# Kernel tuning notes

Hardware: AMD Instinct MI355X
Metric: run time of the kernel (lower is better)

## Reference

```python
import jax, jax.numpy as jnp
import numpy as np

B, N, DIM, H, D = 1, 1024, 512, 8, 64
BC, BS, K, W = 16, 16, 8, 256   # compress blk, selection blk, top-k blocks, sliding window
C = N // BC                     # number of compression / selection blocks
SCALE = D ** -0.5
EPS = 1e-6
NEG = -1e30


def rmsnorm(x):
    return x * jax.lax.rsqrt(jnp.mean(x * x, axis=-1, keepdims=True) + EPS)


def rope(x):  # x: [B,H,N,D], GPT-NeoX style half rotation
    half = D // 2
    inv = 1.0 / (10000.0 ** (jnp.arange(half, dtype=jnp.float32) / half))
    ang = jnp.arange(x.shape[2], dtype=jnp.float32)[:, None] * inv
    cos, sin = jnp.cos(ang), jnp.sin(ang)
    x1, x2 = x[..., :half], x[..., half:]
    return jnp.concatenate([x1 * cos - x2 * sin, x2 * cos + x1 * sin], axis=-1).astype(x.dtype)


def setup_inputs():
    key = jax.random.key(0)
    ks = jax.random.split(key, 24)
    w = lambda k, shape, fan: jax.random.normal(k, shape, jnp.float32) * (fan ** -0.5)
    return {
        'x':  jax.random.normal(ks[0], (B, N, DIM), jnp.float32),
        've': jax.random.normal(ks[1], (B, N, DIM), jnp.float32),
        'x0': jax.random.normal(ks[2], (B, N, DIM), jnp.float32),
        'lambdas': jnp.array([1.0, 0.0], jnp.float32),
        'Wq': w(ks[3], (DIM, H * D), DIM),
        'Wk': w(ks[4], (DIM, H * D), DIM),
        'Wv': w(ks[5], (DIM, H * D), DIM),
        'Wo': w(ks[6], (H * D, DIM), H * D),
        'Wg': w(ks[7], (DIM, 3 * H), DIM),
        'k_pos': w(ks[8], (H, BC, D), D),
        'v_pos': w(ks[9], (H, BC, D), D),
        'Wck': w(ks[10], (BC * D, D), BC * D),
        'bck': jnp.zeros((D,), jnp.float32),
        'Wcv': w(ks[11], (BC * D, D), BC * D),
        'bcv': jnp.zeros((D,), jnp.float32),
        'k_mem': w(ks[12], (H, 1, D), D),
        'v_mem': w(ks[13], (H, 1, D), D),
        'W1': w(ks[14], (DIM, 4 * DIM), DIM),
        'W2': w(ks[15], (4 * DIM, DIM), 4 * DIM),
    }


def _nsa_attn(xn, Wq, Wk, Wv, Wo, Wg, k_pos, v_pos, Wck, bck, Wcv, bcv, k_mem, v_mem):
    q = (xn @ Wq).reshape(B, N, H, D).transpose(0, 2, 1, 3)   # [B,H,N,D]
    k = (xn @ Wk).reshape(B, N, H, D).transpose(0, 2, 1, 3)
    v = (xn @ Wv).reshape(B, N, H, D).transpose(0, 2, 1, 3)
    q, k = rope(q), rope(k)
    i_idx = jnp.arange(N)

    # ---- compressed branch: pool kv into blocks via learned linear + intra-block pos emb ----
    kb = k.reshape(B, H, C, BC, D) + k_pos[None, :, None]
    vb = v.reshape(B, H, C, BC, D) + v_pos[None, :, None]
    ck = kb.reshape(B, H, C, BC * D) @ Wck + bck              # [B,H,C,D]
    cv = vb.reshape(B, H, C, BC * D) @ Wcv + bcv
    ckf = jnp.concatenate([jnp.broadcast_to(k_mem[None], (B, H, 1, D)), ck], axis=2)
    cvf = jnp.concatenate([jnp.broadcast_to(v_mem[None], (B, H, 1, D)), cv], axis=2)
    csim = jnp.einsum('bhid,bhjd->bhij', q, ckf) * SCALE      # [B,H,N,C+1]
    past = ((jnp.arange(C) + 1) * BC - 1)[None, :] < i_idx[:, None]   # block fully in the past
    cmask = jnp.concatenate([jnp.ones((N, 1), bool), past], axis=1)   # mem kv always visible
    cattn = jax.nn.softmax(jnp.where(cmask[None, None], csim, NEG), axis=-1)
    c_out = jnp.einsum('bhij,bhjd->bhid', cattn, cvf)

    # ---- fine selection branch: top-K blocks by compressed attention importance ----
    imp = jnp.where(past[None, None], cattn[..., 1:], NEG)    # [B,H,N,C]
    vals, sel = jax.lax.top_k(imp, K)                         # [B,H,N,K]
    valid = vals >= 0.0                                       # drop picks among masked blocks
    kb_f = k.reshape(B, H, C, BS, D)
    vb_f = v.reshape(B, H, C, BS, D)
    k_sel = jnp.take_along_axis(kb_f[:, :, None], sel[..., None, None], axis=3)  # [B,H,N,K,BS,D]
    v_sel = jnp.take_along_axis(vb_f[:, :, None], sel[..., None, None], axis=3)
    own = i_idx // BS                                         # query's own block, causal inside
    k_fine = jnp.concatenate([k_sel, kb_f[:, :, own][:, :, :, None]], axis=3)    # [B,H,N,K+1,BS,D]
    v_fine = jnp.concatenate([v_sel, vb_f[:, :, own][:, :, :, None]], axis=3)
    offs = jnp.arange(BS)
    m_sel = (sel[..., None] * BS + offs <= i_idx[None, None, :, None, None]) & valid[..., None]
    m_own = jnp.broadcast_to((own[:, None] * BS + offs <= i_idx[:, None])[None, None, :, None], (B, H, N, 1, BS))
    m_fine = jnp.concatenate([m_sel, m_own], axis=3)
    fsim = jnp.where(m_fine, jnp.einsum('bhnd,bhnksd->bhnks', q, k_fine) * SCALE, NEG)
    fattn = jax.nn.softmax(fsim.reshape(B, H, N, (K + 1) * BS), axis=-1).reshape(B, H, N, K + 1, BS)
    f_out = jnp.einsum('bhnks,bhnksd->bhnd', fattn, v_fine)

    # ---- sliding window branch ----
    smask = (i_idx[None, :] <= i_idx[:, None]) & (i_idx[:, None] - i_idx[None, :] < W)
    ssim = jnp.where(smask[None, None], jnp.einsum('bhid,bhjd->bhij', q, k) * SCALE, NEG)
    s_out = jnp.einsum('bhij,bhjd->bhid', jax.nn.softmax(ssim, axis=-1), v)

    # ---- per-head sigmoid gates combine the three strategies ----
    gates = jax.nn.sigmoid(xn @ Wg).reshape(B, N, H, 3).transpose(0, 2, 1, 3)  # [B,H,N,3]
    o = gates[..., 0:1] * c_out + gates[..., 1:2] * f_out + gates[..., 2:3] * s_out
    return o.transpose(0, 2, 1, 3).reshape(B, N, H * D) @ Wo


def reference(x, ve, x0, lambdas, Wq, Wk, Wv, Wo, Wg, k_pos, v_pos, Wck, bck, Wcv, bcv, k_mem, v_mem, W1, W2):
    # ve is accepted by NSABlock.forward but never consumed in this block
    x = lambdas[0] * x + lambdas[1] * x0
    x = x + _nsa_attn(rmsnorm(x), Wq, Wk, Wv, Wo, Wg, k_pos, v_pos, Wck, bck, Wcv, bcv, k_mem, v_mem)
    x = x + jnp.square(jax.nn.relu(rmsnorm(x) @ W1)) @ W2
    return x
```

## Files before the change

### kernel.cpp

```cpp
#include <hip/hip_runtime.h>
#include <math.h>

#define NTOK 1024
#define DIMM 512
#define NH 8
#define HD 64
#define BCB 16
#define BSB 16
#define KSEL 8
#define WWIN 256
#define CBLK 64
#define SCALE 0.125f
#define EPSV 1e-6f
#define NEGV -1e30f

typedef short bf16x8 __attribute__((ext_vector_type(8)));
typedef float f32x4 __attribute__((ext_vector_type(4)));

__device__ inline ushort f2b(float f) {
  union { float f; unsigned int u; } c; c.f = f;
  unsigned int u = c.u;
  return (ushort)((u + 0x7FFFu + ((u >> 16) & 1u)) >> 16);
}
__device__ inline float b2f(ushort h) {
  union { unsigned int u; float f; } c; c.u = ((unsigned int)h) << 16;
  return c.f;
}

__device__ inline float wred_max(float v) {
#pragma unroll
  for (int off = 1; off < 64; off <<= 1) v = fmaxf(v, __shfl_xor(v, off));
  return v;
}
__device__ inline float wred_sum(float v) {
#pragma unroll
  for (int off = 1; off < 64; off <<= 1) v += __shfl_xor(v, off);
  return v;
}

__global__ void __launch_bounds__(256)
k_resid_rms(const float* __restrict__ x, const float* __restrict__ x0,
            const float* __restrict__ lam, float* __restrict__ xr,
            float* __restrict__ xn) {
  int row = blockIdx.x, tid = threadIdx.x;
  float l0 = lam[0], l1 = lam[1];
  size_t b = (size_t)row * DIMM;
  float a0 = l0 * x[b + tid]       + l1 * x0[b + tid];
  float a1 = l0 * x[b + tid + 256] + l1 * x0[b + tid + 256];
  xr[b + tid] = a0; xr[b + tid + 256] = a1;
  float ss = a0 * a0 + a1 * a1;
  __shared__ float sm[8];
  for (int o = 32; o > 0; o >>= 1) ss += __shfl_down(ss, o);
  int lane = tid & 63, wid = tid >> 6;
  if (lane == 0) sm[wid] = ss;
  __syncthreads();
  if (tid == 0) {
    float s = sm[0] + sm[1] + sm[2] + sm[3];
    sm[0] = rsqrtf(s / (float)DIMM + EPSV);
  }
  __syncthreads();
  float r = sm[0];
  xn[b + tid] = a0 * r; xn[b + tid + 256] = a1 * r;
}

__global__ void __launch_bounds__(256)
k_rms_bf(const float* __restrict__ xr, const float* __restrict__ p0,
         const float* __restrict__ p1, float* __restrict__ x2,
         ushort* __restrict__ y) {
  int row = blockIdx.x, tid = threadIdx.x;
  size_t b = (size_t)row * DIMM;
  float a0 = xr[b + tid]       + p0[b + tid]       + p1[b + tid];
  float a1 = xr[b + tid + 256] + p0[b + tid + 256] + p1[b + tid + 256];
  x2[b + tid] = a0; x2[b + tid + 256] = a1;
  float ss = a0 * a0 + a1 * a1;
  __shared__ float sm[8];
  for (int o = 32; o > 0; o >>= 1) ss += __shfl_down(ss, o);
  int lane = tid & 63, wid = tid >> 6;
  if (lane == 0) sm[wid] = ss;
  __syncthreads();
  if (tid == 0) {
    float s = sm[0] + sm[1] + sm[2] + sm[3];
    sm[0] = rsqrtf(s / (float)DIMM + EPSV);
  }
  __syncthreads();
  float r = sm[0];
  y[b + tid] = f2b(a0 * r); y[b + tid + 256] = f2b(a1 * r);
}

struct WtrDesc { const float* src; ushort* dh; ushort* dl; int K; int Nsrc; int Npad; };
struct WtrPack { WtrDesc d[9]; int cum[9]; };

__global__ void __launch_bounds__(256)
k_wtr_all(WtrPack pk) {
  int gb = blockIdx.x;
  int e = 0;
  while (gb >= pk.cum[e]) e++;
  int start = e ? pk.cum[e - 1] : 0;
  WtrDesc dd = pk.d[e];
  int local = gb - start;
  int XT = dd.Npad >> 5;
  int bx = local % XT, by = local / XT;
  __shared__ float t[32][33];
  int n0 = bx * 32, k0 = by * 32;
  int tx = threadIdx.x, ty = threadIdx.y;
#pragma unroll
  for (int i = 0; i < 32; i += 8)
    t[ty + i][tx] = (n0 + tx < dd.Nsrc)
        ? dd.src[(size_t)(k0 + ty + i) * dd.Nsrc + n0 + tx] : 0.f;
  __syncthreads();
#pragma unroll
  for (int i = 0; i < 32; i += 8) {
    float vv = t[tx][ty + i];
    ushort h = f2b(vv);
    size_t di = (size_t)(n0 + ty + i) * dd.K + k0 + tx;
    dd.dh[di] = h;
    if (dd.dl) dd.dl[di] = f2b(vv - b2f(h));
  }
}

__global__ void __launch_bounds__(256)
k_gemm_w1(const ushort* __restrict__ A, const ushort* __restrict__ BT,
          ushort* __restrict__ Co) {
  const int Kd = 512, Nd = 2048;
  __shared__ ushort As[128 * 40];
  __shared__ ushort Bs[64 * 40];
  int tid = threadIdx.x;
  int lane = tid & 63, w = tid >> 6;
  int rb = blockIdx.y * 128, cb = blockIdx.x * 64;
  int wm = (w >> 1) * 64, wn = (w & 1) * 32;
  int quad = lane >> 4, l15 = lane & 15;
  int srA = tid >> 1, scA = (tid & 1) * 16;
  int srB = tid >> 2, scB = (tid & 3) * 8;

  f32x4 acc[4][2];
#pragma unroll
  for (int i = 0; i < 4; i++)
#pragma unroll
    for (int j = 0; j < 2; j++) acc[i][j] = (f32x4){0.f, 0.f, 0.f, 0.f};

  const ushort* ap = A  + (size_t)(rb + srA) * Kd + scA;
  const ushort* bp = BT + (size_t)(cb + srB) * Kd + scB;
  ushort* aw = &As[srA * 40 + scA];
  ushort* bw = &Bs[srB * 40 + scB];

  int4 pa0 = *(const int4*)ap;
  int4 pa1 = *(const int4*)(ap + 8);
  int4 pb  = *(const int4*)bp;

  for (int k0 = 0; k0 < Kd; k0 += 32) {
    if (k0) __syncthreads();
    *(int4*)aw = pa0; *(int4*)(aw + 8) = pa1;
    *(int4*)bw = pb;
    __syncthreads();
    if (k0 + 32 < Kd) {
      pa0 = *(const int4*)(ap + k0 + 32);
      pa1 = *(const int4*)(ap + k0 + 40);
      pb  = *(const int4*)(bp + k0 + 32);
    }
    bf16x8 af[4], bfr[2];
#pragma unroll
    for (int t = 0; t < 4; t++)
      af[t] = *(const bf16x8*)&As[(wm + t * 16 + l15) * 40 + quad * 8];
#pragma unroll
    for (int t = 0; t < 2; t++)
      bfr[t] = *(const bf16x8*)&Bs[(wn + t * 16 + l15) * 40 + quad * 8];
#pragma unroll
    for (int i = 0; i < 4; i++)
#pragma unroll
      for (int j = 0; j < 2; j++)
        acc[i][j] = __builtin_amdgcn_mfma_f32_16x16x32_bf16(af[i], bfr[j],
                                                            acc[i][j], 0, 0, 0);
  }

#pragma unroll
  for (int i = 0; i < 4; i++) {
#pragma unroll
    for (int j = 0; j < 2; j++) {
      int col = cb + wn + j * 16 + l15;
#pragma unroll
      for (int r = 0; r < 4; r++) {
        int row = rb + wm + i * 16 + quad * 4 + r;
        float t = fmaxf(acc[i][j][r], 0.f);
        Co[(size_t)row * Nd + col] = f2b(t * t);
      }
    }
  }
}

__global__ void __launch_bounds__(256)
k_gemm_w2(const ushort* __restrict__ A, const ushort* __restrict__ BT,
          float* __restrict__ P0, float* __restrict__ P1) {
  const int Kd = 2048;
  __shared__ ushort As[64 * 40];
  __shared__ ushort Bs[64 * 40];
  int tid = threadIdx.x;
  int lane = tid & 63, w = tid >> 6;
  int rb = blockIdx.y * 64, cb = blockIdx.x * 64;
  int kb = blockIdx.z * 1024;
  int wm = (w >> 1) * 32, wn = (w & 1) * 32;
  int quad = lane >> 4, l15 = lane & 15;
  int srow = tid >> 2, scol = (tid & 3) * 8;

  f32x4 acc[2][2];
#pragma unroll
  for (int i = 0; i < 2; i++)
#pragma unroll
    for (int j = 0; j < 2; j++) acc[i][j] = (f32x4){0.f, 0.f, 0.f, 0.f};

  const ushort* ap = A  + (size_t)(rb + srow) * Kd + kb + scol;
  const ushort* bp = BT + (size_t)(cb + srow) * Kd + kb + scol;
  ushort* aw = &As[srow * 40 + scol];
  ushort* bw = &Bs[srow * 40 + scol];

  int4 pa = *(const int4*)ap;
  int4 pb = *(const int4*)bp;

  for (int k0 = 0; k0 < 1024; k0 += 32) {
    if (k0) __syncthreads();
    *(int4*)aw = pa;
    *(int4*)bw = pb;
    __syncthreads();
    if (k0 + 32 < 1024) {
      pa = *(const int4*)(ap + k0 + 32);
      pb = *(const int4*)(bp + k0 + 32);
    }
    bf16x8 af[2], bfr[2];
#pragma unroll
    for (int t = 0; t < 2; t++) {
      af[t]  = *(const bf16x8*)&As[(wm + t * 16 + l15) * 40 + quad * 8];
      bfr[t] = *(const bf16x8*)&Bs[(wn + t * 16 + l15) * 40 + quad * 8];
    }
#pragma unroll
    for (int i = 0; i < 2; i++)
#pragma unroll
      for (int j = 0; j < 2; j++)
        acc[i][j] = __builtin_amdgcn_mfma_f32_16x16x32_bf16(af[i], bfr[j],
                                                            acc[i][j], 0, 0, 0);
  }

  float* pbuf = blockIdx.z ? P1 : P0;
#pragma unroll
  for (int i = 0; i < 2; i++) {
#pragma unroll
    for (int j = 0; j < 2; j++) {
      int col = cb + wn + j * 16 + l15;
#pragma unroll
      for (int r = 0; r < 4; r++) {
        int row = rb + wm + i * 16 + quad * 4 + r;
        pbuf[(size_t)row * 512 + col] = acc[i][j][r];
      }
    }
  }
}

__global__ void __launch_bounds__(256)
k_w2fin(const float* __restrict__ x2, const float* __restrict__ p0,
        const float* __restrict__ p1, float* __restrict__ out) {
  int idx = blockIdx.x * 256 + threadIdx.x;
  out[idx] = x2[idx] + p0[idx] + p1[idx];
}

__global__ void __launch_bounds__(256)
k_gemm_wo(const float* __restrict__ cg, const float* __restrict__ fg,
          const float* __restrict__ sg, const float* __restrict__ gates,
          const ushort* __restrict__ BT, float* __restrict__ P0,
          float* __restrict__ P1) {
  __shared__ ushort As[64 * 40];
  __shared__ ushort Bs[64 * 40];
  int tid = threadIdx.x;
  int lane = tid & 63, wave = tid >> 6;
  int rb = blockIdx.y * 64, cb = blockIdx.x * 64;
  int kb = blockIdx.z * 256;
  int wm = (wave >> 1) * 32, wn = (wave & 1) * 32;
  int q = lane >> 4, l15 = lane & 15;
  int srow = tid >> 2, scol = (tid & 3) * 8;

  f32x4 acc[2][2];
#pragma unroll
  for (int i = 0; i < 2; i++)
#pragma unroll
    for (int j = 0; j < 2; j++) acc[i][j] = (f32x4){0.f, 0.f, 0.f, 0.f};

  int row = rb + srow;
  const ushort* bp = BT + (size_t)(cb + srow) * 512 + kb + scol;
  ushort* aw = &As[srow * 40 + scol];
  ushort* bw = &Bs[srow * 40 + scol];

  for (int k0 = 0; k0 < 256; k0 += 32) {
    int colb = kb + k0 + scol;
    int hh = colb >> 6;
    const float* gp = gates + (size_t)row * 24 + hh * 3;
    float g0 = gp[0], g1 = gp[1], g2 = gp[2];
    size_t off = (size_t)row * 512 + colb;
    float4 c0 = *(const float4*)(cg + off), c1 = *(const float4*)(cg + off + 4);
    float4 f0 = *(const float4*)(fg + off), f1 = *(const float4*)(fg + off + 4);
    float4 s0 = *(const float4*)(sg + off), s1 = *(const float4*)(sg + off + 4);
    float va[8] = {g0 * c0.x + g1 * f0.x + g2 * s0.x,
                   g0 * c0.y + g1 * f0.y + g2 * s0.y,
                   g0 * c0.z + g1 * f0.z + g2 * s0.z,
                   g0 * c0.w + g1 * f0.w + g2 * s0.w,
                   g0 * c1.x + g1 * f1.x + g2 * s1.x,
                   g0 * c1.y + g1 * f1.y + g2 * s1.y,
                   g0 * c1.z + g1 * f1.z + g2 * s1.z,
                   g0 * c1.w + g1 * f1.w + g2 * s1.w};
    ushort h[8];
#pragma unroll
    for (int e = 0; e < 8; e++) h[e] = f2b(va[e]);
    *(int4*)aw = *(int4*)h;
    *(int4*)bw = *(const int4*)(bp + k0);
    __syncthreads();
    bf16x8 af[2], bfr[2];
#pragma unroll
    for (int t = 0; t < 2; t++) {
      af[t]  = *(const bf16x8*)&As[(wm + t * 16 + l15) * 40 + q * 8];
      bfr[t] = *(const bf16x8*)&Bs[(wn + t * 16 + l15) * 40 + q * 8];
    }
#pragma unroll
    for (int i = 0; i < 2; i++)
#pragma unroll
      for (int j = 0; j < 2; j++)
        acc[i][j] = __builtin_amdgcn_mfma_f32_16x16x32_bf16(af[i], bfr[j],
                                                            acc[i][j], 0, 0, 0);
    __syncthreads();
  }

  float* pbuf = blockIdx.z ? P1 : P0;
#pragma unroll
  for (int i = 0; i < 2; i++) {
#pragma unroll
    for (int j = 0; j < 2; j++) {
      int col = cb + wn + j * 16 + l15;
#pragma unroll
      for (int r = 0; r < 4; r++) {
        int rr = rb + wm + i * 16 + q * 4 + r;
        pbuf[(size_t)rr * 512 + col] = acc[i][j][r];
      }
    }
  }
}

__global__ void __launch_bounds__(256)
k_gemm_qkv(const float* __restrict__ A, const ushort* __restrict__ BTh,
           const ushort* __restrict__ BTl, float* __restrict__ Co,
           float* __restrict__ vhm, float* __restrict__ gates, int Kd) {
  __shared__ ushort Ash[64 * 40];
  __shared__ ushort Asl[64 * 40];
  __shared__ ushort Bsh[64 * 40];
  __shared__ ushort Bsl[64 * 40];
  int tid = threadIdx.x;
  int lane = tid & 63, wave = tid >> 6;
  int rb = blockIdx.y * 64, cb = blockIdx.x * 64;
  const bool prec = (cb < 1024);
  int wm = (wave >> 1) * 32, wn = (wave & 1) * 32;
  int q = lane >> 4, l15 = lane & 15;
  int srow = tid >> 2, scol = (tid & 3) * 8;

  f32x4 acc[2][2];
#pragma unroll
  for (int i = 0; i < 2; i++)
#pragma unroll
    for (int j = 0; j < 2; j++) acc[i][j] = (f32x4){0.f, 0.f, 0.f, 0.f};

  const float*  ap  = A   + (size_t)(rb + srow) * Kd + scol;
  const ushort* bph = BTh + (size_t)(cb + srow) * Kd + scol;
  const ushort* bpl = BTl + (size_t)(cb + srow) * Kd + scol;
  ushort* awh = &Ash[srow * 40 + scol];
  ushort* awl = &Asl[srow * 40 + scol];
  ushort* bwh = &Bsh[srow * 40 + scol];
  ushort* bwl = &Bsl[srow * 40 + scol];

  for (int k0 = 0; k0 < Kd; k0 += 32) {
    float4 a0 = *(const float4*)(ap + k0);
    float4 a1 = *(const float4*)(ap + k0 + 4);
    float va[8] = {a0.x, a0.y, a0.z, a0.w, a1.x, a1.y, a1.z, a1.w};
    ushort hh[8], hl[8];
#pragma unroll
    for (int e = 0; e < 8; e++) hh[e] = f2b(va[e]);
    *(int4*)awh = *(int4*)hh;
    *(int4*)bwh = *(const int4*)(bph + k0);
    if (prec) {
#pragma unroll
      for (int e = 0; e < 8; e++) hl[e] = f2b(va[e] - b2f(hh[e]));
      *(int4*)awl = *(int4*)hl;
      *(int4*)bwl = *(const int4*)(bpl + k0);
    }
    __syncthreads();
    bf16x8 afh[2], afl[2], bfh[2], bfl[2];
#pragma unroll
    for (int t = 0; t < 2; t++) {
      int ar = (wm + t * 16 + l15) * 40 + q * 8;
      int br = (wn + t * 16 + l15) * 40 + q * 8;
      afh[t] = *(const bf16x8*)&Ash[ar];
      bfh[t] = *(const bf16x8*)&Bsh[br];
      if (prec) {
        afl[t] = *(const bf16x8*)&Asl[ar];
        bfl[t] = *(const bf16x8*)&Bsl[br];
      }
    }
#pragma unroll
    for (int i = 0; i < 2; i++)
#pragma unroll
      for (int j = 0; j < 2; j++) {
        acc[i][j] = __builtin_amdgcn_mfma_f32_16x16x32_bf16(afh[i], bfh[j],
                                                            acc[i][j], 0, 0, 0);
        if (prec) {
          acc[i][j] = __builtin_amdgcn_mfma_f32_16x16x32_bf16(afh[i], bfl[j],
                                                              acc[i][j], 0, 0, 0);
          acc[i][j] = __builtin_amdgcn_mfma_f32_16x16x32_bf16(afl[i], bfh[j],
                                                              acc[i][j], 0, 0, 0);
        }
      }
    __syncthreads();
  }

  const size_t NW = (size_t)NTOK * DIMM;
#pragma unroll
  for (int i = 0; i < 2; i++) {
#pragma unroll
    for (int j = 0; j < 2; j++) {
      int col = cb + wn + j * 16 + l15;
#pragma unroll
      for (int r = 0; r < 4; r++) {
        int row = rb + wm + i * 16 + q * 4 + r;
        float vv = acc[i][j][r];
        if (cb >= 1536) {
          int c24 = col - 1536;
          if (c24 < 24)
            gates[(size_t)row * 24 + c24] = 1.f / (1.f + expf(-vv));
        } else if (col >= 1024) {
          int c = col - 1024;
          vhm[(size_t)(c >> 6) * 65536 + (size_t)row * 64 + (c & 63)] = vv;
        } else {
          Co[(size_t)(col >> 9) * NW + (size_t)row * 512 + (col & 511)] = vv;
        }
      }
    }
  }
}

__global__ void __launch_bounds__(256)
k_rope(float* __restrict__ q, const float* __restrict__ k,
       float* __restrict__ khm, ushort* __restrict__ khm_bf,
       const float* __restrict__ vhm, ushort* __restrict__ vhm_bf) {
  int idx = blockIdx.x * 256 + threadIdx.x;
  int seg = idx >> 18;
  if (seg >= 2) {
    int ci = idx - 524288;
    if (ci < 131072) {
      float4 t = *(const float4*)(vhm + (size_t)ci * 4);
      ushort4 u = {f2b(t.x), f2b(t.y), f2b(t.z), f2b(t.w)};
      *(ushort4*)(vhm_bf + (size_t)ci * 4) = u;
    }
    return;
  }
  int r = idx & 262143;
  int j = r & 31;
  int h = (r >> 5) & 7;
  int n = r >> 8;
  float inv = powf(10000.f, -(float)j / 32.f);
  float ang = (float)n * inv;
  float sn, cs;
  sincosf(ang, &sn, &cs);
  size_t base = (size_t)n * DIMM + h * HD + j;
  if (seg == 0) {
    float x1 = q[base], x2 = q[base + 32];
    q[base] = x1 * cs - x2 * sn;
    q[base + 32] = x2 * cs + x1 * sn;
  } else {
    float x1 = k[base], x2 = k[base + 32];
    float o1 = x1 * cs - x2 * sn;
    float o2 = x2 * cs + x1 * sn;
    size_t ob = (size_t)h * 65536 + (size_t)n * 64 + j;
    khm[ob] = o1;
    khm[ob + 32] = o2;
    khm_bf[ob] = f2b(o1);
    khm_bf[ob + 32] = f2b(o2);
  }
}

__global__ void __launch_bounds__(256)
k_ckcv_m(const float* __restrict__ khm, const float* __restrict__ vhm,
         const float* __restrict__ k_pos, const float* __restrict__ v_pos,
         const ushort* __restrict__ WckTh, const ushort* __restrict__ WckTl,
         const ushort* __restrict__ WcvTh, const ushort* __restrict__ WcvTl,
         const float* __restrict__ bck, const float* __restrict__ bcv,
         float* __restrict__ ckb, float* __restrict__ cvb) {
  int h = blockIdx.x, kv = blockIdx.y, mh = blockIdx.z;
  const float* src = kv ? vhm : khm;
  const float* pos = kv ? v_pos : k_pos;
  const ushort* WTh = kv ? WcvTh : WckTh;
  const ushort* WTl = kv ? WcvTl : WckTl;
  const float* bias = kv ? bcv : bck;
  float* outp = kv ? cvb : ckb;

  __shared__ ushort Ash[32 * 72], Asl[32 * 72];
  __shared__ ushort Bsh[64 * 72], Bsl[64 * 72];
  int tid = threadIdx.x;
  int lane = tid & 63, wave = tid >> 6;
  int wmi = wave >> 1, wnj = wave & 1;
  int quad = lane >> 4, l15 = lane & 15;
  int arow = tid >> 3, ae0 = (tid & 7) * 8;
  int brow = tid >> 2, be0 = (tid & 3) * 16;

  f32x4 acc[2];
#pragma unroll
  for (int j = 0; j < 2; j++) acc[j] = (f32x4){0.f, 0.f, 0.f, 0.f};

  for (int t = 0; t < 16; t++) {
    const float* ar = src + (size_t)h * 65536 +
                      (size_t)((mh * 32 + arow) * 16 + t) * 64 + ae0;
    const float* pr = pos + (size_t)(h * 16 + t) * HD + ae0;
    ushort hh[8], hl[8];
#pragma unroll
    for (int u = 0; u < 2; u++) {
      float4 av = *(const float4*)(ar + u * 4);
      float4 pv = *(const float4*)(pr + u * 4);
      float vals[4] = {av.x + pv.x, av.y + pv.y, av.z + pv.z, av.w + pv.w};
#pragma unroll
      for (int e = 0; e < 4; e++) {
        ushort hb = f2b(vals[e]);
        hh[u * 4 + e] = hb;
        hl[u * 4 + e] = f2b(vals[e] - b2f(hb));
      }
    }
    *(int4*)&Ash[arow * 72 + ae0] = *(int4*)hh;
    *(int4*)&Asl[arow * 72 + ae0] = *(int4*)hl;
    const ushort* bh = WTh + (size_t)brow * 1024 + t * 64 + be0;
    const ushort* bl = WTl + (size_t)brow * 1024 + t * 64 + be0;
    *(int4*)&Bsh[brow * 72 + be0]     = *(const int4*)bh;
    *(int4*)&Bsh[brow * 72 + be0 + 8] = *(const int4*)(bh + 8);
    *(int4*)&Bsl[brow * 72 + be0]     = *(const int4*)bl;
    *(int4*)&Bsl[brow * 72 + be0 + 8] = *(const int4*)(bl + 8);
    __syncthreads();
#pragma unroll
    for (int sub = 0; sub < 2; sub++) {
      int ar2 = (wmi * 16 + l15) * 72 + sub * 32 + quad * 8;
      bf16x8 afh = *(const bf16x8*)&Ash[ar2];
      bf16x8 afl = *(const bf16x8*)&Asl[ar2];
#pragma unroll
      for (int j = 0; j < 2; j++) {
        int br2 = (wnj * 32 + j * 16 + l15) * 72 + sub * 32 + quad * 8;
        bf16x8 bfh = *(const bf16x8*)&Bsh[br2];
        bf16x8 bfl = *(const bf16x8*)&Bsl[br2];
        acc[j] = __builtin_amdgcn_mfma_f32_16x16x32_bf16(afh, bfh, acc[j], 0, 0, 0);
        acc[j] = __builtin_amdgcn_mfma_f32_16x16x32_bf16(afh, bfl, acc[j], 0, 0, 0);
        acc[j] = __builtin_amdgcn_mfma_f32_16x16x32_bf16(afl, bfh, acc[j], 0, 0, 0);
      }
    }
    __syncthreads();
  }

#pragma unroll
  for (int j = 0; j < 2; j++) {
    int d = wnj * 32 + j * 16 + l15;
    float bv = bias[d];
#pragma unroll
    for (int r = 0; r < 4; r++) {
      int c = mh * 32 + wmi * 16 + quad * 4 + r;
      outp[((size_t)h * 64 + c) * 64 + d] = acc[j][r] + bv;
    }
  }
}

__global__ void __launch_bounds__(256)
k_cmp(const float* __restrict__ qg, const float* __restrict__ ckb,
      const float* __restrict__ cvb, const float* __restrict__ k_mem,
      const float* __restrict__ v_mem, float* __restrict__ cout,
      int* __restrict__ sel) {
  int h = blockIdx.y, i0 = blockIdx.x * 16;
  int tid = threadIdx.x, lane = tid & 63, w = tid >> 6;
  __shared__ float ckt[64][65];
  __shared__ float cvs[64][65];
  __shared__ float qs[16][64];
  __shared__ float kms[64], vms[64];
  __shared__ float sp[4][64];

#pragma unroll
  for (int r = 0; r < 4; r++) {
    int f = r * 256 + tid;
    int c = f >> 4, d0 = (f & 15) * 4;
    float4 t = *(const float4*)(ckb + ((size_t)h * 64 + c) * 64 + d0);
    ckt[d0][c] = t.x; ckt[d0 + 1][c] = t.y; ckt[d0 + 2][c] = t.z; ckt[d0 + 3][c] = t.w;
    float4 u = *(const float4*)(cvb + ((size_t)h * 64 + c) * 64 + d0);
    cvs[c][d0] = u.x; cvs[c][d0 + 1] = u.y; cvs[c][d0 + 2] = u.z; cvs[c][d0 + 3] = u.w;
  }
  {
    int r = tid >> 4, d0 = (tid & 15) * 4;
    float4 t = *(const float4*)(qg + (size_t)(i0 + r) * DIMM + h * HD + d0);
    qs[r][d0] = t.x; qs[r][d0 + 1] = t.y; qs[r][d0 + 2] = t.z; qs[r][d0 + 3] = t.w;
  }
  if (tid < 64) kms[tid] = k_mem[h * HD + tid];
  else if (tid < 128) vms[tid - 64] = v_mem[h * HD + tid - 64];
  __syncthreads();

  for (int s = 0; s < 4; s++) {
    int ql = w * 4 + s, qi = i0 + ql;
    float dot = 0.f, dm = 0.f;
#pragma unroll 8
    for (int e = 0; e < 64; e++) {
      float qe = qs[ql][e];
      dot = fmaf(qe, ckt[e][lane], dot);
      dm  = fmaf(qe, kms[e], dm);
    }
    bool vis = (lane * BCB + BCB - 1) < qi;
    float sj = vis ? dot * SCALE : NEGV;
    float smem = dm * SCALE;
    float m = wred_max(fmaxf(sj, smem));
    float p = expf(sj - m);
    float pmem = expf(smem - m);
    float l = wred_sum(p) + pmem;
    float inv = 1.f / l;

    float impv = vis ? p : NEGV;
#pragma unroll
    for (int kk = 0; kk < KSEL; kk++) {
      float bv = impv; int bi = lane;
#pragma unroll
      for (int off = 32; off > 0; off >>= 1) {
        float ov = __shfl_xor(bv, off);
        int   oi = __shfl_xor(bi, off);
        if (ov > bv || (ov == bv && oi < bi)) { bv = ov; bi = oi; }
      }
      if (lane == 0) sel[((size_t)h * NTOK + qi) * KSEL + kk] = (bv >= 0.f) ? bi : -1;
      if (lane == bi) impv = NEGV;
    }

    sp[w][lane] = p;
    float od = pmem * vms[lane];
#pragma unroll 8
    for (int j = 0; j < 64; j++) od = fmaf(sp[w][j], cvs[j][lane], od);
    cout[(size_t)qi * DIMM + h * HD + lane] = od * inv;
  }
}

__global__ void __launch_bounds__(128)
k_swin(const float* __restrict__ qg, const ushort* __restrict__ khm_bf,
       const ushort* __restrict__ vhm_bf, float* __restrict__ sout) {
  int h = blockIdx.y, i0 = blockIdx.x * 32;
  int tid = threadIdx.x, lane = tid & 63, w = tid >> 6;
  int quad = lane >> 4, l15 = lane & 15;

  __shared__ ushort Kt[64 * 72];
  __shared__ ushort VT[64 * 72];
  __shared__ ushort Qs[32 * 72];
  __shared__ ushort Ps[2][16 * 72];

#pragma unroll
  for (int it = 0; it < 2; it++) {
    int f = it * 128 + tid;
    int r = f >> 3, d0 = (f & 7) * 8;
    const float* qp = qg + (size_t)(i0 + r) * DIMM + h * HD + d0;
    float4 t0 = *(const float4*)qp;
    float4 t1 = *(const float4*)(qp + 4);
    ushort u[8] = {f2b(t0.x), f2b(t0.y), f2b(t0.z), f2b(t0.w),
                   f2b(t1.x), f2b(t1.y), f2b(t1.z), f2b(t1.w)};
    *(int4*)&Qs[r * 72 + d0] = *(int4*)u;
  }

  int lo = i0 - (WWIN - 1); if (lo < 0) lo = 0;
  int jb_lo = lo >> 6, jb_hi = (i0 + 31) >> 6;

  float mrow[4], lrow[4];
  f32x4 Of[4];
#pragma unroll
  for (int r = 0; r < 4; r++) { mrow[r] = NEGV; lrow[r] = 0.f; }
#pragma unroll
  for (int d = 0; d < 4; d++) Of[d] = (f32x4){0.f, 0.f, 0.f, 0.f};

  for (int jb = jb_lo; jb <= jb_hi; jb++) {
    __syncthreads();
#pragma unroll
    for (int it = 0; it < 4; it++) {
      int f = it * 128 + tid;
      int r = f >> 3, c8 = (f & 7) * 8;
      const ushort* kp = khm_bf + (size_t)h * 65536 + (size_t)(jb * 64 + r) * 64 + c8;
      *(int4*)&Kt[r * 72 + c8] = *(const int4*)kp;
      const ushort* vp = vhm_bf + (size_t)h * 65536 + (size_t)(jb * 64 + r) * 64 + c8;
      ushort vv[8];
      *(int4*)vv = *(const int4*)vp;
#pragma unroll
      for (int e = 0; e < 8; e++) VT[(c8 + e) * 72 + r] = vv[e];
    }
    __syncthreads();

    bf16x8 qa[2];
#pragma unroll
    for (int c = 0; c < 2; c++)
      qa[c] = *(const bf16x8*)&Qs[(w * 16 + l15) * 72 + c * 32 + quad * 8];

    f32x4 sc[4];
#pragma unroll
    for (int ks = 0; ks < 4; ks++) {
      f32x4 a = (f32x4){0.f, 0.f, 0.f, 0.f};
#pragma unroll
      for (int c = 0; c < 2; c++) {
        bf16x8 kb = *(const bf16x8*)&Kt[(ks * 16 + l15) * 72 + c * 32 + quad * 8];
        a = __builtin_amdgcn_mfma_f32_16x16x32_bf16(qa[c], kb, a, 0, 0, 0);
      }
      sc[ks] = a;
    }

    float pm[4][4], rmax[4];
#pragma unroll
    for (int r = 0; r < 4; r++) rmax[r] = NEGV;
#pragma unroll
    for (int ks = 0; ks < 4; ks++) {
      int gj = jb * 64 + ks * 16 + l15;
#pragma unroll
      for (int r = 0; r < 4; r++) {
        int qi = i0 + w * 16 + quad * 4 + r;
        bool vis = (gj <= qi) && (qi - gj < WWIN);
        float s = vis ? sc[ks][r] * SCALE : NEGV;
        pm[ks][r] = s;
        rmax[r] = fmaxf(rmax[r], s);
      }
    }
#pragma unroll
    for (int off = 1; off < 16; off <<= 1)
#pragma unroll
      for (int r = 0; r < 4; r++)
        rmax[r] = fmaxf(rmax[r], __shfl_xor(rmax[r], off));

    float alpha[4], rsum[4];
#pragma unroll
    for (int r = 0; r < 4; r++) {
      float newm = fmaxf(mrow[r], rmax[r]);
      alpha[r] = expf(mrow[r] - newm);
      mrow[r] = newm;
      rsum[r] = 0.f;
    }
#pragma unroll
    for (int ks = 0; ks < 4; ks++)
#pragma unroll
      for (int r = 0; r < 4; r++) {
        float p = expf(pm[ks][r] - mrow[r]);
        pm[ks][r] = p;
        rsum[r] += p;
      }
#pragma unroll
    for (int off = 1; off < 16; off <<= 1)
#pragma unroll
      for (int r = 0; r < 4; r++)
        rsum[r] += __shfl_xor(rsum[r], off);
#pragma unroll
    for (int r = 0; r < 4; r++)
      lrow[r] = lrow[r] * alpha[r] + rsum[r];

#pragma unroll
    for (int ks = 0; ks < 4; ks++)
#pragma unroll
      for (int r = 0; r < 4; r++)
        Ps[w][(quad * 4 + r) * 72 + ks * 16 + l15] = f2b(pm[ks][r]);
#pragma unroll
    for (int d = 0; d < 4; d++)
#pragma unroll
      for (int r = 0; r < 4; r++)
        Of[d][r] *= alpha[r];

#pragma unroll
    for (int c = 0; c < 2; c++) {
      bf16x8 pa = *(const bf16x8*)&Ps[w][l15 * 72 + c * 32 + quad * 8];
#pragma unroll
      for (int d = 0; d < 4; d++) {
        bf16x8 vb = *(const bf16x8*)&VT[(d * 16 + l15) * 72 + c * 32 + quad * 8];
        Of[d] = __builtin_amdgcn_mfma_f32_16x16x32_bf16(pa, vb, Of[d], 0, 0, 0);
      }
    }
  }

#pragma unroll
  for (int d = 0; d < 4; d++)
#pragma unroll
    for (int r = 0; r < 4; r++) {
      int qi = i0 + w * 16 + quad * 4 + r;
      sout[(size_t)qi * DIMM + h * HD + d * 16 + l15] = Of[d][r] / lrow[r];
    }
}

__global__ void __launch_bounds__(256)
k_fine(const float* __restrict__ qg, const ushort* __restrict__ khm_bf,
       const ushort* __restrict__ vhm_bf, const int* __restrict__ sel,
       float* __restrict__ fout) {
  int i = blockIdx.x, h = blockIdx.y;
  int tid = threadIdx.x, lane = tid & 63, w = tid >> 6;
  __shared__ float qsh[64];
  __shared__ ushort vsb[144 * 64];
  __shared__ float sp[144];
  __shared__ int selS[8];
  __shared__ float mred[4], sredS[4];
  __shared__ float pacc[4][64];

  int own = i >> 4;
  if (tid < 64) qsh[tid] = qg[(size_t)i * DIMM + h * HD + tid];
  if (tid >= 64 && tid < 72)
    selS[tid - 64] = sel[((size_t)h * NTOK + i) * KSEL + tid - 64];
  __syncthreads();

  const ushort* kbase = khm_bf + (size_t)h * 65536;
  const ushort* vbase = vhm_bf + (size_t)h * 65536;

#pragma unroll
  for (int it = 0; it < 5; it++) {
    int idx = it * 256 + tid;
    if (idx < 1152) {
      int row = idx >> 3, c8 = (idx & 7) * 8;
      int kk = row >> 4;
      int bidx = (kk < KSEL) ? selS[kk] : own;
      if (bidx < 0) bidx = 0;
      *(int4*)&vsb[row * 64 + c8] =
          *(const int4*)(vbase + (size_t)(bidx * BSB + (row & 15)) * 64 + c8);
    }
  }

  float s_loc = NEGV;
  bool active = (tid < 144);
  if (active) {
    int kk = tid >> 4;
    int bidx; bool vis;
    if (kk < KSEL) {
      bidx = selS[kk];
      vis = (bidx >= 0);
      if (!vis) bidx = 0;
    } else {
      bidx = own;
      vis = (tid - 128) <= (i & 15);
    }
    const ushort* kr = kbase + (size_t)(bidx * BSB + (tid & 15)) * 64;
    float dot = 0.f;
#pragma unroll
    for (int e8 = 0; e8 < 8; e8++) {
      ushort kv[8];
      *(int4*)kv = *(const int4*)(kr + e8 * 8);
#pragma unroll
      for (int e = 0; e < 8; e++)
        dot = fmaf(qsh[e8 * 8 + e], b2f(kv[e]), dot);
    }
    s_loc = vis ? dot * SCALE : NEGV;
  }
  float mw = wred_max(s_loc);
  if (lane == 0) mred[w] = mw;
  __syncthreads();
  float m = fmaxf(fmaxf(mred[0], mred[1]), fmaxf(mred[2], mred[3]));
  float p = active ? expf(s_loc - m) : 0.f;
  float sw = wred_sum(p);
  if (lane == 0) sredS[w] = sw;
  if (active) sp[tid] = p;
  __syncthreads();
  float l = sredS[0] + sredS[1] + sredS[2] + sredS[3];

  float acc = 0.f;
  int j0 = w * 36;
#pragma unroll 6
  for (int jj = 0; jj < 36; jj++) {
    int j = j0 + jj;
    acc = fmaf(sp[j], b2f(vsb[j * 64 + lane]), acc);
  }
  pacc[w][lane] = acc;
  __syncthreads();
  if (w == 0)
    fout[(size_t)i * DIMM + h * HD + lane] =
        (pacc[0][lane] + pacc[1][lane] + pacc[2][lane] + pacc[3][lane]) / l;
}

extern "C" void kernel_launch(void* const* d_in, const int* in_sizes, int n_in,
                              void* d_out, int out_size, void* d_ws, size_t ws_size,
                              hipStream_t stream) {
  const float* x     = (const float*)d_in[0];
  const float* ve    = (const float*)d_in[1]; (void)ve;
  const float* x0    = (const float*)d_in[2];
  const float* lam   = (const float*)d_in[3];
  const float* Wq    = (const float*)d_in[4];
  const float* Wk    = (const float*)d_in[5];
  const float* Wv    = (const float*)d_in[6];
  const float* Wo    = (const float*)d_in[7];
  const float* Wg    = (const float*)d_in[8];
  const float* k_pos = (const float*)d_in[9];
  const float* v_pos = (const float*)d_in[10];
  const float* Wck   = (const float*)d_in[11];
  const float* bck   = (const float*)d_in[12];
  const float* Wcv   = (const float*)d_in[13];
  const float* bcv   = (const float*)d_in[14];
  const float* k_mem = (const float*)d_in[15];
  const float* v_mem = (const float*)d_in[16];
  const float* W1    = (const float*)d_in[17];
  const float* W2    = (const float*)d_in[18];
  float* out = (float*)d_out;
  float* ws  = (float*)d_ws;

  const size_t NW = (size_t)NTOK * DIMM;
  float* xr    = ws;
  float* xn    = ws + 1 * NW;
  float* q     = ws + 2 * NW;
  float* k     = ws + 3 * NW;
  float* vhm   = ws + 4 * NW;
  float* coutb = ws + 5 * NW;
  float* foutb = ws + 6 * NW;
  float* soutb = ws + 7 * NW;
  float* x2    = ws + 8 * NW;
  float* khm   = x2;
  float* gates = ws + 9 * NW;
  float* ckb   = gates + 32768;
  float* cvb   = ckb + 32768;
  int*   selb  = (int*)(cvb + 32768);
  ushort* qkvTh = (ushort*)(cvb + 32768 + 65536);
  ushort* qkvTl = qkvTh + 1600 * 512;
  ushort* WoT   = qkvTl + 1600 * 512;
  ushort* W1T   = WoT   + 512 * 512;
  ushort* W2T   = W1T   + 2048 * 512;
  ushort* WckTh = W2T   + 512 * 2048;
  ushort* WckTl = WckTh + 64 * 1024;
  ushort* WcvTh = WckTl + 64 * 1024;
  ushort* WcvTl = WcvTh + 64 * 1024;
  float* p0w = k;
  float* p1w = q;
  ushort* ybf = (ushort*)soutb;
  ushort* h1b = (ushort*)q;
  float* p0 = xn;
  float* p1 = vhm;
  ushort* khm_bf = (ushort*)xn;
  ushort* vhm_bf = khm_bf + 524288;

  WtrPack pk;
  pk.d[0] = {Wq, qkvTh,              qkvTl,              512, 512,  512};
  pk.d[1] = {Wk, qkvTh + 512 * 512,  qkvTl + 512 * 512,  512, 512,  512};
  pk.d[2] = {Wv, qkvTh + 1024 * 512, qkvTl + 1024 * 512, 512, 512,  512};
  pk.d[3] = {Wo, WoT, nullptr,  512, 512,  512};
  pk.d[4] = {W1, W1T, nullptr,  512, 2048, 2048};
  pk.d[5] = {W2, W2T, nullptr, 2048, 512,  512};
  pk.d[6] = {Wck, WckTh, WckTl, 1024, 64, 64};
  pk.d[7] = {Wcv, WcvTh, WcvTl, 1024, 64, 64};
  pk.d[8] = {Wg, qkvTh + 1536 * 512, qkvTl + 1536 * 512, 512, 24, 64};
  int cum = 0;
  for (int e = 0; e < 9; e++) {
    cum += (pk.d[e].Npad / 32) * (pk.d[e].K / 32);
    pk.cum[e] = cum;
  }
  k_wtr_all<<<cum, dim3(32, 8), 0, stream>>>(pk);

  k_resid_rms<<<NTOK, 256, 0, stream>>>(x, x0, lam, xr, xn);

  k_gemm_qkv<<<dim3(25, NTOK / 64), 256, 0, stream>>>(
      xn, qkvTh, qkvTl, q, vhm, gates, 512);
  k_rope<<<2560, 256, 0, stream>>>(q, k, khm, khm_bf, vhm, vhm_bf);

  k_ckcv_m<<<dim3(NH, 2, 2), 256, 0, stream>>>(khm, vhm, k_pos, v_pos,
                                               WckTh, WckTl, WcvTh, WcvTl,
                                               bck, bcv, ckb, cvb);
  k_cmp<<<dim3(NTOK / 16, NH), 256, 0, stream>>>(q, ckb, cvb, k_mem, v_mem,
                                                 coutb, selb);
  k_swin<<<dim3(NTOK / 32, NH), 128, 0, stream>>>(q, khm_bf, vhm_bf, soutb);
  k_fine<<<dim3(NTOK, NH), 256, 0, stream>>>(q, khm_bf, vhm_bf, selb, foutb);

  k_gemm_wo<<<dim3(512 / 64, NTOK / 64, 2), 256, 0, stream>>>(
      coutb, foutb, soutb, gates, WoT, p0w, p1w);
  k_rms_bf<<<NTOK, 256, 0, stream>>>(xr, p0w, p1w, x2, ybf);

  k_gemm_w1<<<dim3(2048 / 64, NTOK / 128), 256, 0, stream>>>(ybf, W1T, h1b);
  k_gemm_w2<<<dim3(512 / 64, NTOK / 64, 2), 256, 0, stream>>>(h1b, W2T, p0, p1);
  k_w2fin<<<NW / 256, 256, 0, stream>>>(x2, p0, p1, out);
}
```

Baseline: 270.5 us.

## Merge launches: fuse weight transpose with rmsnorm, ckcv with swin, atomic W2 epilogue

Folds the weight-transpose kernel and the residual rmsnorm into one launch. The rmsnorm now emits bf16 hi/lo splits, so the QKV GEMM no longer converts floats. The compressed-KV projection and the sliding-window attention share one launch (k_mid) through a shared-memory union, and the window kernel now uses 64-query tiles with 4 waves. The W2 GEMM accumulates its split-K halves into the output with atomicAdd on top of the residual written by k_rms_bf, which removes the final add kernel. This cuts launch count and intermediate traffic, at the cost of fewer, larger window blocks and atomic contention.

After: 246.2 us. -9.0%, faster.

```diff
diff --git a/kernel.cpp b/kernel.cpp
--- a/kernel.cpp
+++ b/kernel.cpp
@@ -38,16 +38,74 @@
   return v;
 }
 
+struct WtrDesc { const float* src; ushort* dh; ushort* dl; int K; int Nsrc; int Npad; };
+struct WtrPack { WtrDesc d[9]; int cum[9]; };
+
 __global__ void __launch_bounds__(256)
-k_resid_rms(const float* __restrict__ x, const float* __restrict__ x0,
-            const float* __restrict__ lam, float* __restrict__ xr,
-            float* __restrict__ xn) {
+k_pre(WtrPack pk, const float* __restrict__ x, const float* __restrict__ x0,
+      const float* __restrict__ lam, float* __restrict__ xr,
+      ushort* __restrict__ xnh, ushort* __restrict__ xnl) {
+  if ((int)blockIdx.x < pk.cum[8]) {
+    int gb = blockIdx.x;
+    int e = 0;
+    while (gb >= pk.cum[e]) e++;
+    int start = e ? pk.cum[e - 1] : 0;
+    WtrDesc dd = pk.d[e];
+    int local = gb - start;
+    int XT = dd.Npad >> 5;
+    int bx = local % XT, by = local / XT;
+    __shared__ float t[32][33];
+    int n0 = bx * 32, k0 = by * 32;
+    int tx = threadIdx.x & 31, ty = threadIdx.x >> 5;
+#pragma unroll
+    for (int i = 0; i < 32; i += 8)
+      t[ty + i][tx] = (n0 + tx < dd.Nsrc)
+          ? dd.src[(size_t)(k0 + ty + i) * dd.Nsrc + n0 + tx] : 0.f;
+    __syncthreads();
+#pragma unroll
+    for (int i = 0; i < 32; i += 8) {
+      float vv = t[tx][ty + i];
+      ushort h = f2b(vv);
+      size_t di = (size_t)(n0 + ty + i) * dd.K + k0 + tx;
+      dd.dh[di] = h;
+      if (dd.dl) dd.dl[di] = f2b(vv - b2f(h));
+    }
+  } else {
+    int row = blockIdx.x - pk.cum[8], tid = threadIdx.x;
+    float l0 = lam[0], l1 = lam[1];
+    size_t b = (size_t)row * DIMM;
+    float a0 = l0 * x[b + tid]       + l1 * x0[b + tid];
+    float a1 = l0 * x[b + tid + 256] + l1 * x0[b + tid + 256];
+    xr[b + tid] = a0; xr[b + tid + 256] = a1;
+    float ss = a0 * a0 + a1 * a1;
+    __shared__ float sm[8];
+    for (int o = 32; o > 0; o >>= 1) ss += __shfl_down(ss, o);
+    int lane = tid & 63, wid = tid >> 6;
+    if (lane == 0) sm[wid] = ss;
+    __syncthreads();
+    if (tid == 0) {
+      float s = sm[0] + sm[1] + sm[2] + sm[3];
+      sm[0] = rsqrtf(s / (float)DIMM + EPSV);
+    }
+    __syncthreads();
+    float r = sm[0];
+    float v0 = a0 * r, v1 = a1 * r;
+    ushort h0 = f2b(v0), h1 = f2b(v1);
+    xnh[b + tid] = h0;        xnh[b + tid + 256] = h1;
+    xnl[b + tid] = f2b(v0 - b2f(h0));
+    xnl[b + tid + 256] = f2b(v1 - b2f(h1));
+  }
+}
+
+__global__ void __launch_bounds__(256)
+k_rms_bf(const float* __restrict__ xr, const float* __restrict__ p0,
+         const float* __restrict__ p1, float* __restrict__ outb,
+         ushort* __restrict__ y) {
   int row = blockIdx.x, tid = threadIdx.x;
-  float l0 = lam[0], l1 = lam[1];
   size_t b = (size_t)row * DIMM;
-  float a0 = l0 * x[b + tid]       + l1 * x0[b + tid];
-  float a1 = l0 * x[b + tid + 256] + l1 * x0[b + tid + 256];
-  xr[b + tid] = a0; xr[b + tid + 256] = a1;
+  float a0 = xr[b + tid]       + p0[b + tid]       + p1[b + tid];
+  float a1 = xr[b + tid + 256] + p0[b + tid + 256] + p1[b + tid + 256];
+  outb[b + tid] = a0; outb[b + tid + 256] = a1;
   float ss = a0 * a0 + a1 * a1;
   __shared__ float sm[8];
   for (int o = 32; o > 0; o >>= 1) ss += __shfl_down(ss, o);
@@ -60,62 +118,7 @@
   }
   __syncthreads();
   float r = sm[0];
-  xn[b + tid] = a0 * r; xn[b + tid + 256] = a1 * r;
-}
-
-__global__ void __launch_bounds__(256)
-k_rms_bf(const float* __restrict__ xr, const float* __restrict__ p0,
-         const float* __restrict__ p1, float* __restrict__ x2,
-         ushort* __restrict__ y) {
-  int row = blockIdx.x, tid = threadIdx.x;
-  size_t b = (size_t)row * DIMM;
-  float a0 = xr[b + tid]       + p0[b + tid]       + p1[b + tid];
-  float a1 = xr[b + tid + 256] + p0[b + tid + 256] + p1[b + tid + 256];
-  x2[b + tid] = a0; x2[b + tid + 256] = a1;
-  float ss = a0 * a0 + a1 * a1;
-  __shared__ float sm[8];
-  for (int o = 32; o > 0; o >>= 1) ss += __shfl_down(ss, o);
-  int lane = tid & 63, wid = tid >> 6;
-  if (lane == 0) sm[wid] = ss;
-  __syncthreads();
-  if (tid == 0) {
-    float s = sm[0] + sm[1] + sm[2] + sm[3];
-    sm[0] = rsqrtf(s / (float)DIMM + EPSV);
-  }
-  __syncthreads();
-  float r = sm[0];
   y[b + tid] = f2b(a0 * r); y[b + tid + 256] = f2b(a1 * r);
-}
-
-struct WtrDesc { const float* src; ushort* dh; ushort* dl; int K; int Nsrc; int Npad; };
-struct WtrPack { WtrDesc d[9]; int cum[9]; };
-
-__global__ void __launch_bounds__(256)
-k_wtr_all(WtrPack pk) {
-  int gb = blockIdx.x;
-  int e = 0;
-  while (gb >= pk.cum[e]) e++;
-  int start = e ? pk.cum[e - 1] : 0;
-  WtrDesc dd = pk.d[e];
-  int local = gb - start;
-  int XT = dd.Npad >> 5;
-  int bx = local % XT, by = local / XT;
-  __shared__ float t[32][33];
-  int n0 = bx * 32, k0 = by * 32;
-  int tx = threadIdx.x, ty = threadIdx.y;
-#pragma unroll
-  for (int i = 0; i < 32; i += 8)
-    t[ty + i][tx] = (n0 + tx < dd.Nsrc)
-        ? dd.src[(size_t)(k0 + ty + i) * dd.Nsrc + n0 + tx] : 0.f;
-  __syncthreads();
-#pragma unroll
-  for (int i = 0; i < 32; i += 8) {
-    float vv = t[tx][ty + i];
-    ushort h = f2b(vv);
-    size_t di = (size_t)(n0 + ty + i) * dd.K + k0 + tx;
-    dd.dh[di] = h;
-    if (dd.dl) dd.dl[di] = f2b(vv - b2f(h));
-  }
 }
 
 __global__ void __launch_bounds__(256)
@@ -189,7 +192,7 @@
 
 __global__ void __launch_bounds__(256)
 k_gemm_w2(const ushort* __restrict__ A, const ushort* __restrict__ BT,
-          float* __restrict__ P0, float* __restrict__ P1) {
+          float* __restrict__ outb) {
   const int Kd = 2048;
   __shared__ ushort As[64 * 40];
   __shared__ ushort Bs[64 * 40];
@@ -238,7 +241,6 @@
                                                             acc[i][j], 0, 0, 0);
   }
 
-  float* pbuf = blockIdx.z ? P1 : P0;
 #pragma unroll
   for (int i = 0; i < 2; i++) {
 #pragma unroll
@@ -247,17 +249,10 @@
 #pragma unroll
       for (int r = 0; r < 4; r++) {
         int row = rb + wm + i * 16 + quad * 4 + r;
-        pbuf[(size_t)row * 512 + col] = acc[i][j][r];
-      }
-    }
-  }
-}
-
-__global__ void __launch_bounds__(256)
-k_w2fin(const float* __restrict__ x2, const float* __restrict__ p0,
-        const float* __restrict__ p1, float* __restrict__ out) {
-  int idx = blockIdx.x * 256 + threadIdx.x;
-  out[idx] = x2[idx] + p0[idx] + p1[idx];
+        atomicAdd(&outb[(size_t)row * 512 + col], acc[i][j][r]);
+      }
+    }
+  }
 }
 
 __global__ void __launch_bounds__(256)
@@ -340,9 +335,10 @@
 }
 
 __global__ void __launch_bounds__(256)
-k_gemm_qkv(const float* __restrict__ A, const ushort* __restrict__ BTh,
-           const ushort* __restrict__ BTl, float* __restrict__ Co,
-           float* __restrict__ vhm, float* __restrict__ gates, int Kd) {
+k_gemm_qkv(const ushort* __restrict__ Ah, const ushort* __restrict__ Al,
+           const ushort* __restrict__ BTh, const ushort* __restrict__ BTl,
+           float* __restrict__ Co, float* __restrict__ vhm,
+           float* __restrict__ gates, int Kd) {
   __shared__ ushort Ash[64 * 40];
   __shared__ ushort Asl[64 * 40];
   __shared__ ushort Bsh[64 * 40];
@@ -361,7 +357,8 @@
 #pragma unroll
     for (int j = 0; j < 2; j++) acc[i][j] = (f32x4){0.f, 0.f, 0.f, 0.f};
 
-  const float*  ap  = A   + (size_t)(rb + srow) * Kd + scol;
+  const ushort* aph = Ah  + (size_t)(rb + srow) * Kd + scol;
+  const ushort* apl = Al  + (size_t)(rb + srow) * Kd + scol;
   const ushort* bph = BTh + (size_t)(cb + srow) * Kd + scol;
   const ushort* bpl = BTl + (size_t)(cb + srow) * Kd + scol;
   ushort* awh = &Ash[srow * 40 + scol];
@@ -370,18 +367,10 @@
   ushort* bwl = &Bsl[srow * 40 + scol];
 
   for (int k0 = 0; k0 < Kd; k0 += 32) {
-    float4 a0 = *(const float4*)(ap + k0);
-    float4 a1 = *(const float4*)(ap + k0 + 4);
-    float va[8] = {a0.x, a0.y, a0.z, a0.w, a1.x, a1.y, a1.z, a1.w};
-    ushort hh[8], hl[8];
-#pragma unroll
-    for (int e = 0; e < 8; e++) hh[e] = f2b(va[e]);
-    *(int4*)awh = *(int4*)hh;
+    *(int4*)awh = *(const int4*)(aph + k0);
     *(int4*)bwh = *(const int4*)(bph + k0);
     if (prec) {
-#pragma unroll
-      for (int e = 0; e < 8; e++) hl[e] = f2b(va[e] - b2f(hh[e]));
-      *(int4*)awl = *(int4*)hl;
+      *(int4*)awl = *(const int4*)(apl + k0);
       *(int4*)bwl = *(const int4*)(bpl + k0);
     }
     __syncthreads();
@@ -479,86 +468,231 @@
 }
 
 __global__ void __launch_bounds__(256)
-k_ckcv_m(const float* __restrict__ khm, const float* __restrict__ vhm,
-         const float* __restrict__ k_pos, const float* __restrict__ v_pos,
-         const ushort* __restrict__ WckTh, const ushort* __restrict__ WckTl,
-         const ushort* __restrict__ WcvTh, const ushort* __restrict__ WcvTl,
-         const float* __restrict__ bck, const float* __restrict__ bcv,
-         float* __restrict__ ckb, float* __restrict__ cvb) {
-  int h = blockIdx.x, kv = blockIdx.y, mh = blockIdx.z;
-  const float* src = kv ? vhm : khm;
-  const float* pos = kv ? v_pos : k_pos;
-  const ushort* WTh = kv ? WcvTh : WckTh;
-  const ushort* WTl = kv ? WcvTl : WckTl;
-  const float* bias = kv ? bcv : bck;
-  float* outp = kv ? cvb : ckb;
-
-  __shared__ ushort Ash[32 * 72], Asl[32 * 72];
-  __shared__ ushort Bsh[64 * 72], Bsl[64 * 72];
-  int tid = threadIdx.x;
-  int lane = tid & 63, wave = tid >> 6;
-  int wmi = wave >> 1, wnj = wave & 1;
+k_mid(const float* __restrict__ khm, const float* __restrict__ vhm,
+      const float* __restrict__ k_pos, const float* __restrict__ v_pos,
+      const ushort* __restrict__ WckTh, const ushort* __restrict__ WckTl,
+      const ushort* __restrict__ WcvTh, const ushort* __restrict__ WcvTl,
+      const float* __restrict__ bck, const float* __restrict__ bcv,
+      float* __restrict__ ckb, float* __restrict__ cvb,
+      const float* __restrict__ qg, const ushort* __restrict__ khm_bf,
+      const ushort* __restrict__ vhm_bf, float* __restrict__ sout) {
+  __shared__ union {
+    struct { ushort Ash[32 * 72]; ushort Asl[32 * 72];
+             ushort Bsh[64 * 72]; ushort Bsl[64 * 72]; } c;
+    struct { ushort Kt[64 * 72]; ushort VT[64 * 72];
+             ushort Qs[64 * 72]; ushort Ps[4][16 * 72]; } s;
+  } U;
+  int tid = threadIdx.x, lane = tid & 63, w = tid >> 6;
   int quad = lane >> 4, l15 = lane & 15;
-  int arow = tid >> 3, ae0 = (tid & 7) * 8;
-  int brow = tid >> 2, be0 = (tid & 3) * 16;
-
-  f32x4 acc[2];
-#pragma unroll
-  for (int j = 0; j < 2; j++) acc[j] = (f32x4){0.f, 0.f, 0.f, 0.f};
-
-  for (int t = 0; t < 16; t++) {
-    const float* ar = src + (size_t)h * 65536 +
-                      (size_t)((mh * 32 + arow) * 16 + t) * 64 + ae0;
-    const float* pr = pos + (size_t)(h * 16 + t) * HD + ae0;
-    ushort hh[8], hl[8];
-#pragma unroll
-    for (int u = 0; u < 2; u++) {
-      float4 av = *(const float4*)(ar + u * 4);
-      float4 pv = *(const float4*)(pr + u * 4);
-      float vals[4] = {av.x + pv.x, av.y + pv.y, av.z + pv.z, av.w + pv.w};
-#pragma unroll
-      for (int e = 0; e < 4; e++) {
-        ushort hb = f2b(vals[e]);
-        hh[u * 4 + e] = hb;
-        hl[u * 4 + e] = f2b(vals[e] - b2f(hb));
-      }
-    }
-    *(int4*)&Ash[arow * 72 + ae0] = *(int4*)hh;
-    *(int4*)&Asl[arow * 72 + ae0] = *(int4*)hl;
-    const ushort* bh = WTh + (size_t)brow * 1024 + t * 64 + be0;
-    const ushort* bl = WTl + (size_t)brow * 1024 + t * 64 + be0;
-    *(int4*)&Bsh[brow * 72 + be0]     = *(const int4*)bh;
-    *(int4*)&Bsh[brow * 72 + be0 + 8] = *(const int4*)(bh + 8);
-    *(int4*)&Bsl[brow * 72 + be0]     = *(const int4*)bl;
-    *(int4*)&Bsl[brow * 72 + be0 + 8] = *(const int4*)(bl + 8);
-    __syncthreads();
-#pragma unroll
-    for (int sub = 0; sub < 2; sub++) {
-      int ar2 = (wmi * 16 + l15) * 72 + sub * 32 + quad * 8;
-      bf16x8 afh = *(const bf16x8*)&Ash[ar2];
-      bf16x8 afl = *(const bf16x8*)&Asl[ar2];
-#pragma unroll
-      for (int j = 0; j < 2; j++) {
-        int br2 = (wnj * 32 + j * 16 + l15) * 72 + sub * 32 + quad * 8;
-        bf16x8 bfh = *(const bf16x8*)&Bsh[br2];
-        bf16x8 bfl = *(const bf16x8*)&Bsl[br2];
-        acc[j] = __builtin_amdgcn_mfma_f32_16x16x32_bf16(afh, bfh, acc[j], 0, 0, 0);
-        acc[j] = __builtin_amdgcn_mfma_f32_16x16x32_bf16(afh, bfl, acc[j], 0, 0, 0);
-        acc[j] = __builtin_amdgcn_mfma_f32_16x16x32_bf16(afl, bfh, acc[j], 0, 0, 0);
-      }
-    }
-    __syncthreads();
-  }
-
-#pragma unroll
-  for (int j = 0; j < 2; j++) {
-    int d = wnj * 32 + j * 16 + l15;
-    float bv = bias[d];
-#pragma unroll
-    for (int r = 0; r < 4; r++) {
-      int c = mh * 32 + wmi * 16 + quad * 4 + r;
-      outp[((size_t)h * 64 + c) * 64 + d] = acc[j][r] + bv;
-    }
+
+  if (blockIdx.x < 32) {
+    int h = blockIdx.x & 7, kv = (blockIdx.x >> 3) & 1, mh = blockIdx.x >> 4;
+    const float* src = kv ? vhm : khm;
+    const float* pos = kv ? v_pos : k_pos;
+    const ushort* WTh = kv ? WcvTh : WckTh;
+    const ushort* WTl = kv ? WcvTl : WckTl;
+    const float* bias = kv ? bcv : bck;
+    float* outp = kv ? cvb : ckb;
+
+    ushort* Ash = U.c.Ash; ushort* Asl = U.c.Asl;
+    ushort* Bsh = U.c.Bsh; ushort* Bsl = U.c.Bsl;
+    int wmi = w >> 1, wnj = w & 1;
+    int arow = tid >> 3, ae0 = (tid & 7) * 8;
+    int brow = tid >> 2, be0 = (tid & 3) * 16;
+
+    f32x4 acc[2];
+#pragma unroll
+    for (int j = 0; j < 2; j++) acc[j] = (f32x4){0.f, 0.f, 0.f, 0.f};
+
+    for (int t = 0; t < 16; t++) {
+      const float* ar = src + (size_t)h * 65536 +
+                        (size_t)((mh * 32 + arow) * 16 + t) * 64 + ae0;
+      const float* pr = pos + (size_t)(h * 16 + t) * HD + ae0;
+      ushort hh[8], hl[8];
+#pragma unroll
+      for (int u = 0; u < 2; u++) {
+        float4 av = *(const float4*)(ar + u * 4);
+        float4 pv = *(const float4*)(pr + u * 4);
+        float vals[4] = {av.x + pv.x, av.y + pv.y, av.z + pv.z, av.w + pv.w};
+#pragma unroll
+        for (int e = 0; e < 4; e++) {
+          ushort hb = f2b(vals[e]);
+          hh[u * 4 + e] = hb;
+          hl[u * 4 + e] = f2b(vals[e] - b2f(hb));
+        }
+      }
+      *(int4*)&Ash[arow * 72 + ae0] = *(int4*)hh;
+      *(int4*)&Asl[arow * 72 + ae0] = *(int4*)hl;
+      const ushort* bh = WTh + (size_t)brow * 1024 + t * 64 + be0;
+      const ushort* bl = WTl + (size_t)brow * 1024 + t * 64 + be0;
+      *(int4*)&Bsh[brow * 72 + be0]     = *(const int4*)bh;
+      *(int4*)&Bsh[brow * 72 + be0 + 8] = *(const int4*)(bh + 8);
+      *(int4*)&Bsl[brow * 72 + be0]     = *(const int4*)bl;
+      *(int4*)&Bsl[brow * 72 + be0 + 8] = *(const int4*)(bl + 8);
+      __syncthreads();
+#pragma unroll
+      for (int sub = 0; sub < 2; sub++) {
+        int ar2 = (wmi * 16 + l15) * 72 + sub * 32 + quad * 8;
+        bf16x8 afh = *(const bf16x8*)&Ash[ar2];
+        bf16x8 afl = *(const bf16x8*)&Asl[ar2];
+#pragma unroll
+        for (int j = 0; j < 2; j++) {
+          int br2 = (wnj * 32 + j * 16 + l15) * 72 + sub * 32 + quad * 8;
+          bf16x8 bfh = *(const bf16x8*)&Bsh[br2];
+          bf16x8 bfl = *(const bf16x8*)&Bsl[br2];
+          acc[j] = __builtin_amdgcn_mfma_f32_16x16x32_bf16(afh, bfh, acc[j], 0, 0, 0);
+          acc[j] = __builtin_amdgcn_mfma_f32_16x16x32_bf16(afh, bfl, acc[j], 0, 0, 0);
+          acc[j] = __builtin_amdgcn_mfma_f32_16x16x32_bf16(afl, bfh, acc[j], 0, 0, 0);
+        }
+      }
+      __syncthreads();
+    }
+
+#pragma unroll
+    for (int j = 0; j < 2; j++) {
+      int d = wnj * 32 + j * 16 + l15;
+      float bv = bias[d];
+#pragma unroll
+      for (int r = 0; r < 4; r++) {
+        int c = mh * 32 + wmi * 16 + quad * 4 + r;
+        outp[((size_t)h * 64 + c) * 64 + d] = acc[j][r] + bv;
+      }
+    }
+  } else {
+    int sidx = blockIdx.x - 32;
+    int h = sidx >> 4, i0 = (sidx & 15) * 64;
+    ushort* Kt = U.s.Kt; ushort* VT = U.s.VT; ushort* Qs = U.s.Qs;
+
+#pragma unroll
+    for (int it = 0; it < 2; it++) {
+      int f = it * 256 + tid;
+      int r = f >> 3, d0 = (f & 7) * 8;
+      const float* qp = qg + (size_t)(i0 + r) * DIMM + h * HD + d0;
+      float4 t0 = *(const float4*)qp;
+      float4 t1 = *(const float4*)(qp + 4);
+      ushort u[8] = {f2b(t0.x), f2b(t0.y), f2b(t0.z), f2b(t0.w),
+                     f2b(t1.x), f2b(t1.y), f2b(t1.z), f2b(t1.w)};
+      *(int4*)&Qs[r * 72 + d0] = *(int4*)u;
+    }
+
+    int lo = i0 - (WWIN - 1); if (lo < 0) lo = 0;
+    int jb_lo = lo >> 6, jb_hi = (i0 + 63) >> 6;
+
+    float mrow[4], lrow[4];
+    f32x4 Of[4];
+#pragma unroll
+    for (int r = 0; r < 4; r++) { mrow[r] = NEGV; lrow[r] = 0.f; }
+#pragma unroll
+    for (int d = 0; d < 4; d++) Of[d] = (f32x4){0.f, 0.f, 0.f, 0.f};
+
+    for (int jb = jb_lo; jb <= jb_hi; jb++) {
+      __syncthreads();
+#pragma unroll
+      for (int it = 0; it < 2; it++) {
+        int f = it * 256 + tid;
+        int r = f >> 3, c8 = (f & 7) * 8;
+        const ushort* kp = khm_bf + (size_t)h * 65536 + (size_t)(jb * 64 + r) * 64 + c8;
+        *(int4*)&Kt[r * 72 + c8] = *(const int4*)kp;
+        const ushort* vp = vhm_bf + (size_t)h * 65536 + (size_t)(jb * 64 + r) * 64 + c8;
+        ushort vv[8];
+        *(int4*)vv = *(const int4*)vp;
+#pragma unroll
+        for (int e = 0; e < 8; e++) VT[(c8 + e) * 72 + r] = vv[e];
+      }
+      __syncthreads();
+
+      bf16x8 qa[2];
+#pragma unroll
+      for (int c = 0; c < 2; c++)
+        qa[c] = *(const bf16x8*)&Qs[(w * 16 + l15) * 72 + c * 32 + quad * 8];
+
+      f32x4 sc[4];
+#pragma unroll
+      for (int ks = 0; ks < 4; ks++) {
+        f32x4 a = (f32x4){0.f, 0.f, 0.f, 0.f};
+#pragma unroll
+        for (int c = 0; c < 2; c++) {
+          bf16x8 kb = *(const bf16x8*)&Kt[(ks * 16 + l15) * 72 + c * 32 + quad * 8];
+          a = __builtin_amdgcn_mfma_f32_16x16x32_bf16(qa[c], kb, a, 0, 0, 0);
+        }
+        sc[ks] = a;
+      }
+
+      float pm[4][4], rmax[4];
+#pragma unroll
+      for (int r = 0; r < 4; r++) rmax[r] = NEGV;
+#pragma unroll
+      for (int ks = 0; ks < 4; ks++) {
+        int gj = jb * 64 + ks * 16 + l15;
+#pragma unroll
+        for (int r = 0; r < 4; r++) {
+          int qi = i0 + w * 16 + quad * 4 + r;
+          bool vis = (gj <= qi) && (qi - gj < WWIN);
+          float s = vis ? sc[ks][r] * SCALE : NEGV;
+          pm[ks][r] = s;
+          rmax[r] = fmaxf(rmax[r], s);
+        }
+      }
+#pragma unroll
+      for (int off = 1; off < 16; off <<= 1)
+#pragma unroll
+        for (int r = 0; r < 4; r++)
+          rmax[r] = fmaxf(rmax[r], __shfl_xor(rmax[r], off));
+
+      float alpha[4], rsum[4];
+#pragma unroll
+      for (int r = 0; r < 4; r++) {
+        float newm = fmaxf(mrow[r], rmax[r]);
+        alpha[r] = expf(mrow[r] - newm);
+        mrow[r] = newm;
+        rsum[r] = 0.f;
+      }
+#pragma unroll
+      for (int ks = 0; ks < 4; ks++)
+#pragma unroll
+        for (int r = 0; r < 4; r++) {
+          float p = expf(pm[ks][r] - mrow[r]);
+          pm[ks][r] = p;
+          rsum[r] += p;
+        }
+#pragma unroll
+      for (int off = 1; off < 16; off <<= 1)
+#pragma unroll
+        for (int r = 0; r < 4; r++)
+          rsum[r] += __shfl_xor(rsum[r], off);
+#pragma unroll
+      for (int r = 0; r < 4; r++)
+        lrow[r] = lrow[r] * alpha[r] + rsum[r];
+
+#pragma unroll
+      for (int ks = 0; ks < 4; ks++)
+#pragma unroll
+        for (int r = 0; r < 4; r++)
+          U.s.Ps[w][(quad * 4 + r) * 72 + ks * 16 + l15] = f2b(pm[ks][r]);
+#pragma unroll
+      for (int d = 0; d < 4; d++)
+#pragma unroll
+        for (int r = 0; r < 4; r++)
+          Of[d][r] *= alpha[r];
+
+#pragma unroll
+      for (int c = 0; c < 2; c++) {
+        bf16x8 pa = *(const bf16x8*)&U.s.Ps[w][l15 * 72 + c * 32 + quad * 8];
+#pragma unroll
+        for (int d = 0; d < 4; d++) {
+          bf16x8 vb = *(const bf16x8*)&VT[(d * 16 + l15) * 72 + c * 32 + quad * 8];
+          Of[d] = __builtin_amdgcn_mfma_f32_16x16x32_bf16(pa, vb, Of[d], 0, 0, 0);
+        }
+      }
+    }
+
+#pragma unroll
+    for (int d = 0; d < 4; d++)
+#pragma unroll
+      for (int r = 0; r < 4; r++) {
+        int qi = i0 + w * 16 + quad * 4 + r;
+        sout[(size_t)qi * DIMM + h * HD + d * 16 + l15] = Of[d][r] / lrow[r];
+      }
   }
 }
 
@@ -631,150 +765,6 @@
     for (int j = 0; j < 64; j++) od = fmaf(sp[w][j], cvs[j][lane], od);
     cout[(size_t)qi * DIMM + h * HD + lane] = od * inv;
   }
-}
-
-__global__ void __launch_bounds__(128)
-k_swin(const float* __restrict__ qg, const ushort* __restrict__ khm_bf,
-       const ushort* __restrict__ vhm_bf, float* __restrict__ sout) {
-  int h = blockIdx.y, i0 = blockIdx.x * 32;
-  int tid = threadIdx.x, lane = tid & 63, w = tid >> 6;
-  int quad = lane >> 4, l15 = lane & 15;
-
-  __shared__ ushort Kt[64 * 72];
-  __shared__ ushort VT[64 * 72];
-  __shared__ ushort Qs[32 * 72];
-  __shared__ ushort Ps[2][16 * 72];
-
-#pragma unroll
-  for (int it = 0; it < 2; it++) {
-    int f = it * 128 + tid;
-    int r = f >> 3, d0 = (f & 7) * 8;
-    const float* qp = qg + (size_t)(i0 + r) * DIMM + h * HD + d0;
-    float4 t0 = *(const float4*)qp;
-    float4 t1 = *(const float4*)(qp + 4);
-    ushort u[8] = {f2b(t0.x), f2b(t0.y), f2b(t0.z), f2b(t0.w),
-                   f2b(t1.x), f2b(t1.y), f2b(t1.z), f2b(t1.w)};
-    *(int4*)&Qs[r * 72 + d0] = *(int4*)u;
-  }
-
-  int lo = i0 - (WWIN - 1); if (lo < 0) lo = 0;
-  int jb_lo = lo >> 6, jb_hi = (i0 + 31) >> 6;
-
-  float mrow[4], lrow[4];
-  f32x4 Of[4];
-#pragma unroll
-  for (int r = 0; r < 4; r++) { mrow[r] = NEGV; lrow[r] = 0.f; }
-#pragma unroll
-  for (int d = 0; d < 4; d++) Of[d] = (f32x4){0.f, 0.f, 0.f, 0.f};
-
-  for (int jb = jb_lo; jb <= jb_hi; jb++) {
-    __syncthreads();
-#pragma unroll
-    for (int it = 0; it < 4; it++) {
-      int f = it * 128 + tid;
-      int r = f >> 3, c8 = (f & 7) * 8;
-      const ushort* kp = khm_bf + (size_t)h * 65536 + (size_t)(jb * 64 + r) * 64 + c8;
-      *(int4*)&Kt[r * 72 + c8] = *(const int4*)kp;
-      const ushort* vp = vhm_bf + (size_t)h * 65536 + (size_t)(jb * 64 + r) * 64 + c8;
-      ushort vv[8];
-      *(int4*)vv = *(const int4*)vp;
-#pragma unroll
-      for (int e = 0; e < 8; e++) VT[(c8 + e) * 72 + r] = vv[e];
-    }
-    __syncthreads();
-
-    bf16x8 qa[2];
-#pragma unroll
-    for (int c = 0; c < 2; c++)
-      qa[c] = *(const bf16x8*)&Qs[(w * 16 + l15) * 72 + c * 32 + quad * 8];
-
-    f32x4 sc[4];
-#pragma unroll
-    for (int ks = 0; ks < 4; ks++) {
-      f32x4 a = (f32x4){0.f, 0.f, 0.f, 0.f};
-#pragma unroll
-      for (int c = 0; c < 2; c++) {
-        bf16x8 kb = *(const bf16x8*)&Kt[(ks * 16 + l15) * 72 + c * 32 + quad * 8];
-        a = __builtin_amdgcn_mfma_f32_16x16x32_bf16(qa[c], kb, a, 0, 0, 0);
-      }
-      sc[ks] = a;
-    }
-
-    float pm[4][4], rmax[4];
-#pragma unroll
-    for (int r = 0; r < 4; r++) rmax[r] = NEGV;
-#pragma unroll
-    for (int ks = 0; ks < 4; ks++) {
-      int gj = jb * 64 + ks * 16 + l15;
-#pragma unroll
-      for (int r = 0; r < 4; r++) {
-        int qi = i0 + w * 16 + quad * 4 + r;
-        bool vis = (gj <= qi) && (qi - gj < WWIN);
-        float s = vis ? sc[ks][r] * SCALE : NEGV;
-        pm[ks][r] = s;
-        rmax[r] = fmaxf(rmax[r], s);
-      }
-    }
-#pragma unroll
-    for (int off = 1; off < 16; off <<= 1)
-#pragma unroll
-      for (int r = 0; r < 4; r++)
-        rmax[r] = fmaxf(rmax[r], __shfl_xor(rmax[r], off));
-
-    float alpha[4], rsum[4];
-#pragma unroll
-    for (int r = 0; r < 4; r++) {
-      float newm = fmaxf(mrow[r], rmax[r]);
-      alpha[r] = expf(mrow[r] - newm);
-      mrow[r] = newm;
-      rsum[r] = 0.f;
-    }
-#pragma unroll
-    for (int ks = 0; ks < 4; ks++)
-#pragma unroll
-      for (int r = 0; r < 4; r++) {
-        float p = expf(pm[ks][r] - mrow[r]);
-        pm[ks][r] = p;
-        rsum[r] += p;
-      }
-#pragma unroll
-    for (int off = 1; off < 16; off <<= 1)
-#pragma unroll
-      for (int r = 0; r < 4; r++)
-        rsum[r] += __shfl_xor(rsum[r], off);
-#pragma unroll
-    for (int r = 0; r < 4; r++)
-      lrow[r] = lrow[r] * alpha[r] + rsum[r];
-
-#pragma unroll
-    for (int ks = 0; ks < 4; ks++)
-#pragma unroll
-      for (int r = 0; r < 4; r++)
-        Ps[w][(quad * 4 + r) * 72 + ks * 16 + l15] = f2b(pm[ks][r]);
-#pragma unroll
-    for (int d = 0; d < 4; d++)
-#pragma unroll
-      for (int r = 0; r < 4; r++)
-        Of[d][r] *= alpha[r];
-
-#pragma unroll
-    for (int c = 0; c < 2; c++) {
-      bf16x8 pa = *(const bf16x8*)&Ps[w][l15 * 72 + c * 32 + quad * 8];
-#pragma unroll
-      for (int d = 0; d < 4; d++) {
-        bf16x8 vb = *(const bf16x8*)&VT[(d * 16 + l15) * 72 + c * 32 + quad * 8];
-        Of[d] = __builtin_amdgcn_mfma_f32_16x16x32_bf16(pa, vb, Of[d], 0, 0, 0);
-      }
-    }
-  }
-
-#pragma unroll
-  for (int d = 0; d < 4; d++)
-#pragma unroll
-    for (int r = 0; r < 4; r++) {
-      int qi = i0 + w * 16 + quad * 4 + r;
-      sout[(size_t)qi * DIMM + h * HD + d * 16 + l15] = Of[d][r] / lrow[r];
-    }
 }
 
 __global__ void __launch_bounds__(256)
@@ -896,8 +886,7 @@
   float* coutb = ws + 5 * NW;
   float* foutb = ws + 6 * NW;
   float* soutb = ws + 7 * NW;
-  float* x2    = ws + 8 * NW;
-  float* khm   = x2;
+  float* khm   = ws + 8 * NW;
   float* gates = ws + 9 * NW;
   float* ckb   = gates + 32768;
   float* cvb   = ckb + 32768;
@@ -915,8 +904,8 @@
   float* p1w = q;
   ushort* ybf = (ushort*)soutb;
   ushort* h1b = (ushort*)q;
-  float* p0 = xn;
-  float* p1 = vhm;
+  ushort* xnh = (ushort*)xn;
+  ushort* xnl = xnh + NW;
   ushort* khm_bf = (ushort*)xn;
   ushort* vhm_bf = khm_bf + 524288;
 
@@ -935,27 +924,26 @@
     cum += (pk.d[e].Npad / 32) * (pk.d[e].K / 32);
     pk.cum[e] = cum;
   }
-  k_wtr_all<<<cum, dim3(32, 8), 0, stream>>>(pk);
-
-  k_resid_rms<<<NTOK, 256, 0, stream>>>(x, x0, lam, xr, xn);
+
+  k_pre<<<cum + NTOK, 256, 0, stream>>>(pk, x, x0, lam, xr, xnh, xnl);
 
   k_gemm_qkv<<<dim3(25, NTOK / 64), 256, 0, stream>>>(
-      xn, qkvTh, qkvTl, q, vhm, gates, 512);
+      xnh, xnl, qkvTh, qkvTl, q, vhm, gates, 512);
   k_rope<<<2560, 256, 0, stream>>>(q, k, khm, khm_bf, vhm, vhm_bf);
 
-  k_ckcv_m<<<dim3(NH, 2, 2), 256, 0, stream>>>(khm, vhm, k_pos, v_pos,
-                                               WckTh, WckTl, WcvTh, WcvTl,
-                                               bck, bcv, ckb, cvb);
+  k_mid<<<160, 256, 0, stream>>>(khm, vhm, k_pos, v_pos,
+                                 WckTh, WckTl, WcvTh, WcvTl,
+                                 bck, bcv, ckb, cvb,
+                                 q, khm_bf, vhm_bf, soutb);
+
   k_cmp<<<dim3(NTOK / 16, NH), 256, 0, stream>>>(q, ckb, cvb, k_mem, v_mem,
                                                  coutb, selb);
-  k_swin<<<dim3(NTOK / 32, NH), 128, 0, stream>>>(q, khm_bf, vhm_bf, soutb);
   k_fine<<<dim3(NTOK, NH), 256, 0, stream>>>(q, khm_bf, vhm_bf, selb, foutb);
 
   k_gemm_wo<<<dim3(512 / 64, NTOK / 64, 2), 256, 0, stream>>>(
       coutb, foutb, soutb, gates, WoT, p0w, p1w);
-  k_rms_bf<<<NTOK, 256, 0, stream>>>(xr, p0w, p1w, x2, ybf);
+  k_rms_bf<<<NTOK, 256, 0, stream>>>(xr, p0w, p1w, out, ybf);
 
   k_gemm_w1<<<dim3(2048 / 64, NTOK / 128), 256, 0, stream>>>(ybf, W1T, h1b);
-  k_gemm_w2<<<dim3(512 / 64, NTOK / 64, 2), 256, 0, stream>>>(h1b, W2T, p0, p1);
-  k_w2fin<<<NW / 256, 256, 0, stream>>>(x2, p0, p1, out);
-}
+  k_gemm_w2<<<dim3(512 / 64, NTOK / 64, 2), 256, 0, stream>>>(h1b, W2T, out);
+}
```
